# Optimization experiments

Measured on AMD Instinct MI355X. Metric: run time of the kernel, lower is better.

## Reference

```python
import jax, jax.numpy as jnp
import numpy as np

B, IN, OUT, P, NS = 256, 1024, 512, 1000, 128

def setup_inputs() -> dict:
    key = jax.random.key(0)
    ks = jax.random.split(key, 6)
    return {
        "x": jax.random.normal(ks[0], (B, IN), jnp.float32),
        "noise": jax.random.normal(ks[1], (B, NS, P), jnp.float32),
        "fb_w": jax.random.normal(ks[2], (1, IN), jnp.float32) * (1.0 / np.sqrt(IN)),
        "fb_b": jnp.zeros((1,), jnp.float32),
        "decay_param": jnp.full((1,), 0.1, jnp.float32),
        "conv_w": jax.random.normal(ks[3], (P, P, 3), jnp.float32) * (1.0 / np.sqrt(3 * P)),
        "conv_b": jnp.zeros((P,), jnp.float32),
        "out_w": jax.random.normal(ks[4], (OUT, P), jnp.float32) * (1.0 / np.sqrt(P)),
        "out_b": jnp.zeros((OUT,), jnp.float32),
    }


def reference(x, noise, fb_w, fb_b, decay_param, conv_w, conv_b, out_w, out_b):
    # x: [B, IN]; noise: [B, NS, P] (Brownian increments for the SDE kernel)
    n_steps = noise.shape[1]
    dt = 1.0 / n_steps                       # T = 1.0
    sd = jnp.sqrt(jnp.asarray(dt, x.dtype))
    # per-sample feedback value: sigmoid(feedback_controller(x))
    feedback = jax.nn.sigmoid(x @ fb_w.T + fb_b)            # [B, 1]
    # decay value: sigmoid(decay_controller) * 0.5 (scalar)
    decay = jax.nn.sigmoid(decay_param[0]) * 0.5
    retain = 1.0 - decay * dt
    # Batched Euler-Maruyama Brownian SDE: X_{t+1} = (1 - decay*dt) X_t + feedback*sqrt(dt)*eps_t
    eps = jnp.transpose(noise, (1, 0, 2))                    # [NS, B, P]
    x0 = jnp.zeros((x.shape[0], noise.shape[2]), x.dtype)

    def step(X, e):
        Xn = X * retain + feedback * sd * e
        return Xn, Xn

    _, paths = jax.lax.scan(step, x0, eps)                   # [NS, B, P]
    paths_bct = jnp.transpose(paths, (1, 2, 0))              # [B, P, NS]
    # temporal_aggregator: Conv1d(P, P, kernel=3, padding=1) over time, then mean over time
    agg = jax.lax.conv_general_dilated(
        paths_bct, conv_w, window_strides=(1,), padding=[(1, 1)],
        dimension_numbers=("NCH", "OIH", "NCH"))
    agg = (agg + conv_b[None, :, None]).mean(axis=2)         # [B, P]
    # output_projection: P -> OUT
    return agg @ out_w.T + out_b
```

## Files before the change

kernel.cpp:

```cpp
#include <hip/hip_runtime.h>
#include <hip/hip_bf16.h>

#define B_N   256
#define IN_N  1024
#define OUT_N 512
#define P_N   1000
#define NS_N  128

#define K1P   3072
#define N1P   1024
#define K2P   1024
#define SK1   16
#define SK2   16

typedef __attribute__((ext_vector_type(8))) short short8v;
typedef __attribute__((ext_vector_type(4))) float f32x4;
typedef unsigned short ushort_t;
typedef __attribute__((ext_vector_type(4))) unsigned short ushort4v;

__device__ __forceinline__ float sigmoid_f(float z) { return 1.0f / (1.0f + __expf(-z)); }

__device__ __forceinline__ ushort_t f2bf(float x) {
    return __bfloat16_as_ushort(__float2bfloat16(x));
}
__device__ __forceinline__ float bf2f(ushort_t h) {
    union { unsigned u; float f; } v; v.u = ((unsigned)h) << 16;
    return v.f;
}

__global__ __launch_bounds__(512) void sde_fused_kernel(const float* __restrict__ x,
                                                        const float* __restrict__ fb_w,
                                                        const float* __restrict__ fb_b,
                                                        const float* __restrict__ noise,
                                                        const float* __restrict__ decay_param,
                                                        ushort_t* __restrict__ Thi) {
    const int b  = blockIdx.x;
    const int ch = blockIdx.y;
    const int t  = threadIdx.x;
    const int cg = t & 127;
    const int tq = t >> 7;

    float2 xv = ((const float2*)(x + (size_t)b * IN_N))[t];
    float2 wv = ((const float2*)fb_w)[t];
    float partial = xv.x * wv.x + xv.y * wv.y;
    #pragma unroll
    for (int o = 32; o >= 1; o >>= 1) partial += __shfl_down(partial, o, 64);
    __shared__ float wred[8];
    if ((t & 63) == 0) wred[t >> 6] = partial;
    __syncthreads();
    float fbs = wred[0] + wred[1] + wred[2] + wred[3] +
                wred[4] + wred[5] + wred[6] + wred[7];
    float fbv = sigmoid_f(fbs + fb_b[0]);

    float decay = sigmoid_f(decay_param[0]) * 0.5f;
    const float dt = 1.0f / NS_N;
    float retain = 1.0f - decay * dt;
    float inv_omr = 1.0f / (decay * dt);
    float r2 = retain * retain, r4 = r2 * r2, r8 = r4 * r4;
    float r16 = r8 * r8, r32 = r16 * r16;
    float r64 = r32 * r32, r96 = r64 * r32;

    const int c0 = ch * 512 + cg * 4;
    const bool act = (c0 < P_N);
    const float* base = noise + (size_t)b * NS_N * P_N + (act ? c0 : 0);

    float4 sE = {0, 0, 0, 0}, L = {0, 0, 0, 0};
    if (act) {
        const int s0 = tq * 32;
        float rp = 1.0f;
        #pragma unroll 8
        for (int ss = s0 + 31; ss >= s0; --ss) {
            float4 e = *(const float4*)(base + (size_t)ss * P_N);
            sE.x += e.x; sE.y += e.y; sE.z += e.z; sE.w += e.w;
            L.x += rp * e.x; L.y += rp * e.y; L.z += rp * e.z; L.w += rp * e.w;
            rp *= retain;
        }
    }

    __shared__ float4 xSE[3][128], xL[3][128], xF[128];
    if (tq < 3) { xSE[tq][cg] = sE; xL[tq][cg] = L; }
    if (tq == 0 && act) xF[cg] = *(const float4*)base;
    __syncthreads();

    if (tq == 3) {
        size_t tb = (size_t)b * K1P + 3 * (size_t)c0;
        if (!act) {
            #pragma unroll
            for (int j = 0; j < 12; ++j) Thi[tb + j] = 0;
            return;
        }
        float4 se0 = xSE[0][cg], se1 = xSE[1][cg], se2 = xSE[2][cg];
        float4 l0 = xL[0][cg], l1 = xL[1][cg], l2 = xL[2][cg], ff = xF[cg];
        float Se[4] = {se0.x + se1.x + se2.x + sE.x, se0.y + se1.y + se2.y + sE.y,
                       se0.z + se1.z + se2.z + sE.z, se0.w + se1.w + se2.w + sE.w};
        float Lv[4] = {L.x + r32 * l2.x + r64 * l1.x + r96 * l0.x,
                       L.y + r32 * l2.y + r64 * l1.y + r96 * l0.y,
                       L.z + r32 * l2.z + r64 * l1.z + r96 * l0.z,
                       L.w + r32 * l2.w + r64 * l1.w + r96 * l0.w};
        float Fv[4] = {ff.x, ff.y, ff.z, ff.w};
        float sd = sqrtf(dt);
        float scale = fbv * sd * (1.0f / NS_N);
        #pragma unroll
        for (int j = 0; j < 4; ++j) {
            float Aj = (Se[j] - retain * Lv[j]) * inv_omr;
            Thi[tb + 3 * j + 0] = f2bf(scale * (Aj - Lv[j]));
            Thi[tb + 3 * j + 1] = f2bf(scale * Aj);
            Thi[tb + 3 * j + 2] = f2bf(scale * (Aj - Fv[j]));
        }
    }
}

__global__ __launch_bounds__(512) void gemm_bf16_bm256(const ushort_t* __restrict__ A,
                                                       const float* __restrict__ B,
                                                       ushort_t* __restrict__ Cpart,
                                                       int lda, int ldb,
                                                       int Nvalid, int Kvalid,
                                                       int Kper, int ldc) {
    __shared__ __align__(16) ushort_t As[256 * 64];
    __shared__ __align__(16) ushort_t Bs[128 * 64];

    const int tid  = threadIdx.x;
    const int lane = tid & 63;
    const int wave = tid >> 6;
    const int r15  = lane & 15;
    const int g4   = lane >> 4;
    const int wrow = wave >> 1;
    const int wcol = wave & 1;
    const int n0 = blockIdx.x * 128;
    const int kbeg = blockIdx.z * Kper;

    f32x4 acc[4][4] = {};

    for (int kt = 0; kt < Kper; kt += 64) {
        const int kk0 = kbeg + kt;
        #pragma unroll
        for (int c = 0; c < 4; ++c) {
            int ci = c * 512 + tid;
            int row = ci >> 3;
            int gs  = ci & 7;
            int g   = gs ^ (row & 7);
            const ushort_t* src = A + (size_t)row * lda + kk0 + g * 8;
            __builtin_amdgcn_global_load_lds(
                (const __attribute__((address_space(1))) void*)src,
                (__attribute__((address_space(3))) void*)&As[(size_t)(c * 512 + wave * 64) * 8],
                16, 0, 0);
        }
        #pragma unroll
        for (int c = 0; c < 2; ++c) {
            int chunk = tid + c * 512;
            int row = chunk >> 3, g = chunk & 7;
            int ldsoff = row * 64 + ((g ^ (row & 7)) << 3);
            int k = kk0 + g * 8;
            short8v bh = {0, 0, 0, 0, 0, 0, 0, 0};
            if ((n0 + row) < Nvalid && k < Kvalid) {
                const float* bp = B + (size_t)(n0 + row) * ldb + k;
                float4 b0 = *(const float4*)bp;
                float4 b1 = *(const float4*)(bp + 4);
                bh[0] = (short)f2bf(b0.x); bh[1] = (short)f2bf(b0.y);
                bh[2] = (short)f2bf(b0.z); bh[3] = (short)f2bf(b0.w);
                bh[4] = (short)f2bf(b1.x); bh[5] = (short)f2bf(b1.y);
                bh[6] = (short)f2bf(b1.z); bh[7] = (short)f2bf(b1.w);
            }
            *(short8v*)&Bs[ldsoff] = bh;
        }
        __syncthreads();

        #pragma unroll
        for (int ks = 0; ks < 2; ++ks) {
            const int g = ks * 4 + g4;
            short8v af[4], bfv[4];
            #pragma unroll
            for (int f = 0; f < 4; ++f) {
                int arow = wrow * 64 + f * 16 + r15;
                af[f] = *(const short8v*)&As[arow * 64 + ((g ^ (arow & 7)) << 3)];
            }
            #pragma unroll
            for (int f = 0; f < 4; ++f) {
                int brow = wcol * 64 + f * 16 + r15;
                bfv[f] = *(const short8v*)&Bs[brow * 64 + ((g ^ (brow & 7)) << 3)];
            }
            #pragma unroll
            for (int mf = 0; mf < 4; ++mf) {
                #pragma unroll
                for (int nf = 0; nf < 4; ++nf) {
                    acc[mf][nf] = __builtin_amdgcn_mfma_f32_16x16x32_bf16(af[mf], bfv[nf], acc[mf][nf], 0, 0, 0);
                }
            }
        }
        __syncthreads();
    }

    ushort_t* cp = Cpart + (size_t)blockIdx.z * B_N * ldc;
    #pragma unroll
    for (int mf = 0; mf < 4; ++mf) {
        #pragma unroll
        for (int nf = 0; nf < 4; ++nf) {
            #pragma unroll
            for (int r = 0; r < 4; ++r) {
                int m = wrow * 64 + mf * 16 + g4 * 4 + r;
                int n = n0 + wcol * 64 + nf * 16 + r15;
                cp[(size_t)m * ldc + n] = f2bf(acc[mf][nf][r]);
            }
        }
    }
}

__global__ __launch_bounds__(256) void reduce_agg_kernel(const ushort_t* __restrict__ Cpart1,
                                                         const float* __restrict__ conv_b,
                                                         ushort_t* __restrict__ agg) {
    int idx4 = (blockIdx.x * 256 + threadIdx.x) * 4;
    int n = idx4 & (N1P - 1);
    float s0 = 0.f, s1 = 0.f, s2 = 0.f, s3 = 0.f;
    if (n < P_N) {
        float4 cb = *(const float4*)(conv_b + n);
        s0 = cb.x; s1 = cb.y; s2 = cb.z; s3 = cb.w;
        #pragma unroll
        for (int z = 0; z < SK1; ++z) {
            ushort4v p = *(const ushort4v*)(Cpart1 + (size_t)z * (B_N * N1P) + idx4);
            s0 += bf2f(p[0]); s1 += bf2f(p[1]); s2 += bf2f(p[2]); s3 += bf2f(p[3]);
        }
    }
    ushort4v o = {f2bf(s0), f2bf(s1), f2bf(s2), f2bf(s3)};
    *(ushort4v*)(agg + idx4) = o;
}

__global__ __launch_bounds__(256) void reduce_out_kernel(const ushort_t* __restrict__ Cpart2,
                                                         const float* __restrict__ out_b,
                                                         float* __restrict__ out) {
    int idx4 = (blockIdx.x * 256 + threadIdx.x) * 4;
    int n = idx4 & (OUT_N - 1);
    float4 ob = *(const float4*)(out_b + n);
    float s0 = ob.x, s1 = ob.y, s2 = ob.z, s3 = ob.w;
    #pragma unroll
    for (int z = 0; z < SK2; ++z) {
        ushort4v p = *(const ushort4v*)(Cpart2 + (size_t)z * (B_N * OUT_N) + idx4);
        s0 += bf2f(p[0]); s1 += bf2f(p[1]); s2 += bf2f(p[2]); s3 += bf2f(p[3]);
    }
    float4 o = {s0, s1, s2, s3};
    *(float4*)(out + idx4) = o;
}

extern "C" void kernel_launch(void* const* d_in, const int* in_sizes, int n_in,
                              void* d_out, int out_size, void* d_ws, size_t ws_size,
                              hipStream_t stream) {
    const float* x           = (const float*)d_in[0];
    const float* noise       = (const float*)d_in[1];
    const float* fb_w        = (const float*)d_in[2];
    const float* fb_b        = (const float*)d_in[3];
    const float* decay_param = (const float*)d_in[4];
    const float* conv_w      = (const float*)d_in[5];
    const float* conv_b      = (const float*)d_in[6];
    const float* out_w       = (const float*)d_in[7];
    const float* out_b       = (const float*)d_in[8];
    float* out = (float*)d_out;

    char* ws = (char*)d_ws;
    size_t off = 0;
    ushort_t* Thi    = (ushort_t*)(ws + off); off += (size_t)B_N * K1P * 2;
    ushort_t* agg    = (ushort_t*)(ws + off); off += (size_t)B_N * K2P * 2;
    ushort_t* Cpart1 = (ushort_t*)(ws + off); off += (size_t)SK1 * B_N * N1P * 2;
    ushort_t* Cpart2 = (ushort_t*)(ws + off); off += (size_t)SK2 * B_N * OUT_N * 2;

    {
        dim3 grid(B_N, 2);
        sde_fused_kernel<<<grid, 512, 0, stream>>>(x, fb_w, fb_b, noise, decay_param, Thi);
    }

    {
        dim3 grid(N1P / 128, 1, SK1);
        gemm_bf16_bm256<<<grid, 512, 0, stream>>>(Thi, conv_w, Cpart1,
                                                  K1P, 3 * P_N, P_N, 3 * P_N,
                                                  K1P / SK1, N1P);
    }

    reduce_agg_kernel<<<(B_N * N1P) / 1024, 256, 0, stream>>>(Cpart1, conv_b, agg);

    {
        dim3 grid(OUT_N / 128, 1, SK2);
        gemm_bf16_bm256<<<grid, 512, 0, stream>>>(agg, out_w, Cpart2,
                                                  K2P, P_N, OUT_N, P_N,
                                                  K2P / SK2, OUT_N);
    }

    reduce_out_kernel<<<(B_N * OUT_N) / 1024, 256, 0, stream>>>(Cpart2, out_b, out);
}
```

Before: 45.96 us.

## Fuse split-K reductions into GEMM kernels via atomic counter barriers

The two separate split-K reduction kernels are removed. Each GEMM block now writes its partial tile, arrives on a per-column-tile atomic counter, spins until all split-K slices are done, and then reduces a 16-row slice of the tile, adding the bias. This saves two kernel launches and their launch gaps. It relies on all blocks of the grid being co-resident (128 and 64 blocks) and adds spin-wait and fence overhead. Counters are zeroed in the SDE kernel.

Result: slower. 101.5 us (+120.8%).

```diff
diff --git a/kernel.cpp b/kernel.cpp
--- a/kernel.cpp
+++ b/kernel.cpp
@@ -33,12 +33,15 @@
                                                         const float* __restrict__ fb_b,
                                                         const float* __restrict__ noise,
                                                         const float* __restrict__ decay_param,
-                                                        ushort_t* __restrict__ Thi) {
+                                                        ushort_t* __restrict__ Thi,
+                                                        int* __restrict__ cnt) {
     const int b  = blockIdx.x;
     const int ch = blockIdx.y;
     const int t  = threadIdx.x;
     const int cg = t & 127;
     const int tq = t >> 7;
+
+    if (b == 0 && ch == 0 && t < 12) cnt[t] = 0;
 
     float2 xv = ((const float2*)(x + (size_t)b * IN_N))[t];
     float2 wv = ((const float2*)fb_w)[t];
@@ -110,12 +113,24 @@
     }
 }
 
-__global__ __launch_bounds__(512) void gemm_bf16_bm256(const ushort_t* __restrict__ A,
-                                                       const float* __restrict__ B,
-                                                       ushort_t* __restrict__ Cpart,
-                                                       int lda, int ldb,
-                                                       int Nvalid, int Kvalid,
-                                                       int Kper, int ldc) {
+__device__ __forceinline__ void arrive_and_wait(int* cnt_slot, int target, int tid) {
+    __threadfence();
+    __syncthreads();
+    if (tid == 0) {
+        atomicAdd(cnt_slot, 1);
+        while (__hip_atomic_load(cnt_slot, __ATOMIC_ACQUIRE, __HIP_MEMORY_SCOPE_AGENT) < target) {
+            __builtin_amdgcn_s_sleep(2);
+        }
+    }
+    __syncthreads();
+}
+
+__global__ __launch_bounds__(512) void gemm1_fused(const ushort_t* __restrict__ A,
+                                                   const float* __restrict__ B,
+                                                   ushort_t* __restrict__ Cpart,
+                                                   const float* __restrict__ conv_b,
+                                                   ushort_t* __restrict__ agg,
+                                                   int* __restrict__ cnt) {
     __shared__ __align__(16) ushort_t As[256 * 64];
     __shared__ __align__(16) ushort_t Bs[128 * 64];
 
@@ -127,11 +142,12 @@
     const int wrow = wave >> 1;
     const int wcol = wave & 1;
     const int n0 = blockIdx.x * 128;
-    const int kbeg = blockIdx.z * Kper;
+    const int z  = blockIdx.z;
+    const int kbeg = z * (K1P / SK1);
 
     f32x4 acc[4][4] = {};
 
-    for (int kt = 0; kt < Kper; kt += 64) {
+    for (int kt = 0; kt < K1P / SK1; kt += 64) {
         const int kk0 = kbeg + kt;
         #pragma unroll
         for (int c = 0; c < 4; ++c) {
@@ -139,7 +155,7 @@
             int row = ci >> 3;
             int gs  = ci & 7;
             int g   = gs ^ (row & 7);
-            const ushort_t* src = A + (size_t)row * lda + kk0 + g * 8;
+            const ushort_t* src = A + (size_t)row * K1P + kk0 + g * 8;
             __builtin_amdgcn_global_load_lds(
                 (const __attribute__((address_space(1))) void*)src,
                 (__attribute__((address_space(3))) void*)&As[(size_t)(c * 512 + wave * 64) * 8],
@@ -152,8 +168,8 @@
             int ldsoff = row * 64 + ((g ^ (row & 7)) << 3);
             int k = kk0 + g * 8;
             short8v bh = {0, 0, 0, 0, 0, 0, 0, 0};
-            if ((n0 + row) < Nvalid && k < Kvalid) {
-                const float* bp = B + (size_t)(n0 + row) * ldb + k;
+            if ((n0 + row) < P_N && k < 3 * P_N) {
+                const float* bp = B + (size_t)(n0 + row) * (3 * P_N) + k;
                 float4 b0 = *(const float4*)bp;
                 float4 b1 = *(const float4*)(bp + 4);
                 bh[0] = (short)f2bf(b0.x); bh[1] = (short)f2bf(b0.y);
@@ -190,7 +206,7 @@
         __syncthreads();
     }
 
-    ushort_t* cp = Cpart + (size_t)blockIdx.z * B_N * ldc;
+    ushort_t* cp = Cpart + (size_t)z * (B_N * N1P);
     #pragma unroll
     for (int mf = 0; mf < 4; ++mf) {
         #pragma unroll
@@ -199,45 +215,140 @@
             for (int r = 0; r < 4; ++r) {
                 int m = wrow * 64 + mf * 16 + g4 * 4 + r;
                 int n = n0 + wcol * 64 + nf * 16 + r15;
-                cp[(size_t)m * ldc + n] = f2bf(acc[mf][nf][r]);
-            }
-        }
-    }
-}
-
-__global__ __launch_bounds__(256) void reduce_agg_kernel(const ushort_t* __restrict__ Cpart1,
-                                                         const float* __restrict__ conv_b,
-                                                         ushort_t* __restrict__ agg) {
-    int idx4 = (blockIdx.x * 256 + threadIdx.x) * 4;
-    int n = idx4 & (N1P - 1);
-    float s0 = 0.f, s1 = 0.f, s2 = 0.f, s3 = 0.f;
-    if (n < P_N) {
-        float4 cb = *(const float4*)(conv_b + n);
-        s0 = cb.x; s1 = cb.y; s2 = cb.z; s3 = cb.w;
-        #pragma unroll
-        for (int z = 0; z < SK1; ++z) {
-            ushort4v p = *(const ushort4v*)(Cpart1 + (size_t)z * (B_N * N1P) + idx4);
+                cp[(size_t)m * N1P + n] = f2bf(acc[mf][nf][r]);
+            }
+        }
+    }
+
+    arrive_and_wait(&cnt[blockIdx.x], SK1, tid);
+
+    {
+        int row = z * 16 + (tid >> 5);
+        int n   = n0 + ((tid & 31) << 2);
+        float s0 = 0.f, s1 = 0.f, s2 = 0.f, s3 = 0.f;
+        if (n < P_N) {
+            float4 cb = *(const float4*)(conv_b + n);
+            s0 = cb.x; s1 = cb.y; s2 = cb.z; s3 = cb.w;
+            size_t o = (size_t)row * N1P + n;
+            #pragma unroll
+            for (int zz = 0; zz < SK1; ++zz) {
+                ushort4v p = *(const ushort4v*)(Cpart + (size_t)zz * (B_N * N1P) + o);
+                s0 += bf2f(p[0]); s1 += bf2f(p[1]); s2 += bf2f(p[2]); s3 += bf2f(p[3]);
+            }
+        }
+        ushort4v ov = {f2bf(s0), f2bf(s1), f2bf(s2), f2bf(s3)};
+        *(ushort4v*)(agg + (size_t)row * K2P + n) = ov;
+    }
+}
+
+__global__ __launch_bounds__(512) void gemm2_fused(const ushort_t* __restrict__ agg,
+                                                   const float* __restrict__ B,
+                                                   ushort_t* __restrict__ Cpart,
+                                                   const float* __restrict__ out_b,
+                                                   float* __restrict__ out,
+                                                   int* __restrict__ cnt) {
+    __shared__ __align__(16) ushort_t As[256 * 64];
+    __shared__ __align__(16) ushort_t Bs[128 * 64];
+
+    const int tid  = threadIdx.x;
+    const int lane = tid & 63;
+    const int wave = tid >> 6;
+    const int r15  = lane & 15;
+    const int g4   = lane >> 4;
+    const int wrow = wave >> 1;
+    const int wcol = wave & 1;
+    const int n0 = blockIdx.x * 128;
+    const int z  = blockIdx.z;
+    const int kk0 = z * 64;
+
+    f32x4 acc[4][4] = {};
+
+    #pragma unroll
+    for (int c = 0; c < 4; ++c) {
+        int ci = c * 512 + tid;
+        int row = ci >> 3;
+        int gs  = ci & 7;
+        int g   = gs ^ (row & 7);
+        const ushort_t* src = agg + (size_t)row * K2P + kk0 + g * 8;
+        __builtin_amdgcn_global_load_lds(
+            (const __attribute__((address_space(1))) void*)src,
+            (__attribute__((address_space(3))) void*)&As[(size_t)(c * 512 + wave * 64) * 8],
+            16, 0, 0);
+    }
+    #pragma unroll
+    for (int c = 0; c < 2; ++c) {
+        int chunk = tid + c * 512;
+        int row = chunk >> 3, g = chunk & 7;
+        int ldsoff = row * 64 + ((g ^ (row & 7)) << 3);
+        int k = kk0 + g * 8;
+        short8v bh = {0, 0, 0, 0, 0, 0, 0, 0};
+        if (k < P_N) {
+            const float* bp = B + (size_t)(n0 + row) * P_N + k;
+            float4 b0 = *(const float4*)bp;
+            float4 b1 = *(const float4*)(bp + 4);
+            bh[0] = (short)f2bf(b0.x); bh[1] = (short)f2bf(b0.y);
+            bh[2] = (short)f2bf(b0.z); bh[3] = (short)f2bf(b0.w);
+            bh[4] = (short)f2bf(b1.x); bh[5] = (short)f2bf(b1.y);
+            bh[6] = (short)f2bf(b1.z); bh[7] = (short)f2bf(b1.w);
+        }
+        *(short8v*)&Bs[ldsoff] = bh;
+    }
+    __syncthreads();
+
+    #pragma unroll
+    for (int ks = 0; ks < 2; ++ks) {
+        const int g = ks * 4 + g4;
+        short8v af[4], bfv[4];
+        #pragma unroll
+        for (int f = 0; f < 4; ++f) {
+            int arow = wrow * 64 + f * 16 + r15;
+            af[f] = *(const short8v*)&As[arow * 64 + ((g ^ (arow & 7)) << 3)];
+        }
+        #pragma unroll
+        for (int f = 0; f < 4; ++f) {
+            int brow = wcol * 64 + f * 16 + r15;
+            bfv[f] = *(const short8v*)&Bs[brow * 64 + ((g ^ (brow & 7)) << 3)];
+        }
+        #pragma unroll
+        for (int mf = 0; mf < 4; ++mf) {
+            #pragma unroll
+            for (int nf = 0; nf < 4; ++nf) {
+                acc[mf][nf] = __builtin_amdgcn_mfma_f32_16x16x32_bf16(af[mf], bfv[nf], acc[mf][nf], 0, 0, 0);
+            }
+        }
+    }
+    __syncthreads();
+
+    ushort_t* cp = Cpart + (size_t)z * (B_N * OUT_N);
+    #pragma unroll
+    for (int mf = 0; mf < 4; ++mf) {
+        #pragma unroll
+        for (int nf = 0; nf < 4; ++nf) {
+            #pragma unroll
+            for (int r = 0; r < 4; ++r) {
+                int m = wrow * 64 + mf * 16 + g4 * 4 + r;
+                int n = n0 + wcol * 64 + nf * 16 + r15;
+                cp[(size_t)m * OUT_N + n] = f2bf(acc[mf][nf][r]);
+            }
+        }
+    }
+
+    arrive_and_wait(&cnt[blockIdx.x], SK2, tid);
+
+    {
+        int row = z * 16 + (tid >> 5);
+        int n   = n0 + ((tid & 31) << 2);
+        float4 ob = *(const float4*)(out_b + n);
+        float s0 = ob.x, s1 = ob.y, s2 = ob.z, s3 = ob.w;
+        size_t o = (size_t)row * OUT_N + n;
+        #pragma unroll
+        for (int zz = 0; zz < SK2; ++zz) {
+            ushort4v p = *(const ushort4v*)(Cpart + (size_t)zz * (B_N * OUT_N) + o);
             s0 += bf2f(p[0]); s1 += bf2f(p[1]); s2 += bf2f(p[2]); s3 += bf2f(p[3]);
         }
-    }
-    ushort4v o = {f2bf(s0), f2bf(s1), f2bf(s2), f2bf(s3)};
-    *(ushort4v*)(agg + idx4) = o;
-}
-
-__global__ __launch_bounds__(256) void reduce_out_kernel(const ushort_t* __restrict__ Cpart2,
-                                                         const float* __restrict__ out_b,
-                                                         float* __restrict__ out) {
-    int idx4 = (blockIdx.x * 256 + threadIdx.x) * 4;
-    int n = idx4 & (OUT_N - 1);
-    float4 ob = *(const float4*)(out_b + n);
-    float s0 = ob.x, s1 = ob.y, s2 = ob.z, s3 = ob.w;
-    #pragma unroll
-    for (int z = 0; z < SK2; ++z) {
-        ushort4v p = *(const ushort4v*)(Cpart2 + (size_t)z * (B_N * OUT_N) + idx4);
-        s0 += bf2f(p[0]); s1 += bf2f(p[1]); s2 += bf2f(p[2]); s3 += bf2f(p[3]);
-    }
-    float4 o = {s0, s1, s2, s3};
-    *(float4*)(out + idx4) = o;
+        float4 ov = {s0, s1, s2, s3};
+        *(float4*)(out + o) = ov;
+    }
 }
 
 extern "C" void kernel_launch(void* const* d_in, const int* in_sizes, int n_in,
@@ -260,27 +371,20 @@
     ushort_t* agg    = (ushort_t*)(ws + off); off += (size_t)B_N * K2P * 2;
     ushort_t* Cpart1 = (ushort_t*)(ws + off); off += (size_t)SK1 * B_N * N1P * 2;
     ushort_t* Cpart2 = (ushort_t*)(ws + off); off += (size_t)SK2 * B_N * OUT_N * 2;
+    int*      cnt    = (int*)(ws + off);      off += 64;
 
     {
         dim3 grid(B_N, 2);
-        sde_fused_kernel<<<grid, 512, 0, stream>>>(x, fb_w, fb_b, noise, decay_param, Thi);
+        sde_fused_kernel<<<grid, 512, 0, stream>>>(x, fb_w, fb_b, noise, decay_param, Thi, cnt);
     }
 
     {
         dim3 grid(N1P / 128, 1, SK1);
-        gemm_bf16_bm256<<<grid, 512, 0, stream>>>(Thi, conv_w, Cpart1,
-                                                  K1P, 3 * P_N, P_N, 3 * P_N,
-                                                  K1P / SK1, N1P);
-    }
-
-    reduce_agg_kernel<<<(B_N * N1P) / 1024, 256, 0, stream>>>(Cpart1, conv_b, agg);
+        gemm1_fused<<<grid, 512, 0, stream>>>(Thi, conv_w, Cpart1, conv_b, agg, cnt);
+    }
 
     {
         dim3 grid(OUT_N / 128, 1, SK2);
-        gemm_bf16_bm256<<<grid, 512, 0, stream>>>(agg, out_w, Cpart2,
-                                                  K2P, P_N, OUT_N, P_N,
-                                                  K2P / SK2, OUT_N);
-    }
-
-    reduce_out_kernel<<<(B_N * OUT_N) / 1024, 256, 0, stream>>>(Cpart2, out_b, out);
-}
+        gemm2_fused<<<grid, 512, 0, stream>>>(agg, out_w, Cpart2, out_b, out, cnt + 8);
+    }
+}
```
